# Optimization experiments

Measured on AMD Instinct MI355X. Metric: run time of the kernel, lower is better.

The kernel has to match this reference:

```python
import jax, jax.numpy as jnp
import numpy as np
from jax import lax

STRIDE = 2
PADDING = 3
NUM_ROW = 8192
NUM_COL = 8192
KH, KW = 7, 7


def setup_inputs() -> dict:
    key = jax.random.key(0)
    kx, kw_, kb = jax.random.split(key, 3)
    enc_x = jax.random.normal(kx, (NUM_ROW * NUM_COL,), dtype=jnp.float32)
    weight = jax.random.normal(kw_, (1, 1, KH, KW), dtype=jnp.float32)
    bias = jax.random.normal(kb, (1,), dtype=jnp.float32)
    return {
        "enc_x": enc_x,
        "weight": weight,
        "bias": bias,
        "num_row": NUM_ROW,
        "num_col": NUM_COL,
    }


def reference(enc_x, weight, bias, num_row, num_col):
    # enc_x is the flattened (packed) image vector of a num_row x num_col image.
    # The CKKS Conv2dFunction computes a plain single-channel cross-correlation
    # (same semantics as torch Conv2d, 1 in / 1 out channel) + scalar bias,
    # returning the flattened output vector.
    x = enc_x.reshape(1, 1, num_row, num_col)  # NCHW
    out = lax.conv_general_dilated(
        x,
        weight,  # OIHW
        window_strides=(STRIDE, STRIDE),
        padding=[(PADDING, PADDING), (PADDING, PADDING)],
        dimension_numbers=("NCHW", "OIHW", "NCHW"),
    )
    out = out + bias[0]
    return out.reshape(-1)  # flattened, matching ciphertext packing
```

## Files before the change

kernel.cpp:

```cpp
#include <hip/hip_runtime.h>


#define THREADS 256
#define TILE_W 128
#define TILE_H 16
#define IN_H 37
#define CHUNKS 66
#define LDS_STRIDE (CHUNKS * 4)
#define NSLOT (IN_H * CHUNKS)
#define NSLOT_PAD 2560
#define IMG 8192
#define OUTW 4096

typedef __attribute__((address_space(1))) const void global_cv;
typedef __attribute__((address_space(3))) void lds_v;

__global__ __launch_bounds__(THREADS, 4)
void conv7x7_s2(const float* __restrict__ x, const float* __restrict__ wgt,
                const float* __restrict__ bias, float* __restrict__ out) {
  __shared__ __align__(16) float lds[NSLOT_PAD * 4];
  const int t = threadIdx.x;
  const int tile_x = blockIdx.x * TILE_W;
  const int tile_y = blockIdx.y * TILE_H;
  const int g0c4 = tile_x * 2 - 4;
  const int g0r = tile_y * 2 - 3;

  float wv[49];
#pragma unroll
  for (int i = 0; i < 49; ++i) wv[i] = wgt[i];
  const float bv = bias[0];

  const bool interior = (blockIdx.x >= 1) & (blockIdx.x <= 30) &
                        (blockIdx.y >= 1) & (blockIdx.y <= 254);

  if (interior) {
    const float* xb = x + (long long)g0r * IMG + g0c4;
#pragma unroll
    for (int i = 0; i < 10; ++i) {
      const int s = t + THREADS * i;
      const int r = s / CHUNKS;
      const int q = s - r * CHUNKS;
      const int xr = (r >> 2) & 7;
      const int src = (q < 64) ? (q ^ xr) : q;
      const float* gp = xb + r * IMG + 4 * src;
      if (i == 9 && s >= NSLOT) gp = x;
      __builtin_amdgcn_global_load_lds((global_cv*)gp, (lds_v*)&lds[s * 4],
                                       16, 0, 0);
    }
  } else {
    float4 vbuf[10];
    int laddr[10];
#pragma unroll
    for (int i = 0; i < 10; ++i) {
      const int s = t + THREADS * i;
      const bool ok = (s < NSLOT);
      const int r = s / CHUNKS;
      const int q = s - r * CHUNKS;
      const int xr = (r >> 2) & 7;
      const int src = (q < 64) ? (q ^ xr) : q;
      const int gr = g0r + r;
      const int gc = g0c4 + 4 * src;
      float4 v = make_float4(0.f, 0.f, 0.f, 0.f);
      if (ok && (unsigned)gr < (unsigned)IMG && (unsigned)gc < (unsigned)(IMG - 3))
        v = *reinterpret_cast<const float4*>(&x[(long long)gr * IMG + gc]);
      vbuf[i] = v;
      laddr[i] = ok ? s * 4 : -1;
    }
#pragma unroll
    for (int i = 0; i < 10; ++i)
      if (laddr[i] >= 0) *reinterpret_cast<float4*>(&lds[laddr[i]]) = vbuf[i];
  }
  __syncthreads();

  const int tx = t & 31;
  const int ty = t >> 5;
  float acc[2][4];
#pragma unroll
  for (int y = 0; y < 2; ++y)
#pragma unroll
    for (int xx = 0; xx < 4; ++xx) acc[y][xx] = bv;

#pragma unroll
  for (int j = 0; j < 9; ++j) {
    const int sl = 4 * ty + j;
    const int xr = (sl >> 2) & 7;
    float rbuf[16];
#pragma unroll
    for (int q = 0; q < 4; ++q) {
      const int c = 2 * tx + q;
      const int lq = (c < 64) ? (c ^ xr) : c;
      const float4 v =
          *reinterpret_cast<const float4*>(&lds[sl * LDS_STRIDE + lq * 4]);
      rbuf[4 * q + 0] = v.x;
      rbuf[4 * q + 1] = v.y;
      rbuf[4 * q + 2] = v.z;
      rbuf[4 * q + 3] = v.w;
    }
#pragma unroll
    for (int y = 0; y < 2; ++y) {
      const int kh = j - 2 * y;
      if (kh >= 0 && kh <= 6) {
#pragma unroll
        for (int xx = 0; xx < 4; ++xx)
#pragma unroll
          for (int kw = 0; kw < 7; ++kw)
            acc[y][xx] = fmaf(rbuf[2 * xx + kw + 1], wv[kh * 7 + kw], acc[y][xx]);
      }
    }
  }

  const int ox = tile_x + 4 * tx;
  const int oy = tile_y + 2 * ty;
#pragma unroll
  for (int y = 0; y < 2; ++y) {
    float4 v = make_float4(acc[y][0], acc[y][1], acc[y][2], acc[y][3]);
    *reinterpret_cast<float4*>(&out[(long long)(oy + y) * OUTW + ox]) = v;
  }
}

extern "C" void kernel_launch(void* const* d_in, const int* in_sizes, int n_in,
                              void* d_out, int out_size, void* d_ws, size_t ws_size,
                              hipStream_t stream) {
  const float* x = (const float*)d_in[0];
  const float* w = (const float*)d_in[1];
  const float* b = (const float*)d_in[2];
  float* out = (float*)d_out;
  dim3 grid(OUTW / TILE_W, OUTW / TILE_H);
  conv7x7_s2<<<grid, dim3(THREADS), 0, stream>>>(x, w, b, out);
}
```

Baseline: 67.00 us.

## Widen conv tile to 256x8 and store LDS chunks even/odd split

Changes the output tile from 128x16 to 256x8 per block, which shrinks the input halo rows loaded per block (21 rows instead of 37 for half as many output rows) and widens each row. The LDS layout replaces the XOR swizzle with a split of even and odd 16-byte chunks into separate halves of each row, so each thread's four float4 reads are consecutive across lanes and avoid bank conflicts without swizzle arithmetic. LDS use per block grows and the occupancy hint drops from 4 to 3 blocks per SIMD-group, trading some latency hiding for less redundant halo traffic.

```diff
diff --git a/kernel.cpp b/kernel.cpp
--- a/kernel.cpp
+++ b/kernel.cpp
@@ -2,20 +2,21 @@
 
 
 #define THREADS 256
-#define TILE_W 128
-#define TILE_H 16
-#define IN_H 37
-#define CHUNKS 66
-#define LDS_STRIDE (CHUNKS * 4)
+#define TILE_W 256
+#define TILE_H 8
+#define IN_H 21
+#define CHUNKS 130
+#define ROWF (CHUNKS * 4)
 #define NSLOT (IN_H * CHUNKS)
-#define NSLOT_PAD 2560
+#define NROUND 11
+#define NSLOT_PAD (NROUND * THREADS)
 #define IMG 8192
 #define OUTW 4096
 
 typedef __attribute__((address_space(1))) const void global_cv;
 typedef __attribute__((address_space(3))) void lds_v;
 
-__global__ __launch_bounds__(THREADS, 4)
+__global__ __launch_bounds__(THREADS, 3)
 void conv7x7_s2(const float* __restrict__ x, const float* __restrict__ wgt,
                 const float* __restrict__ bias, float* __restrict__ out) {
   __shared__ __align__(16) float lds[NSLOT_PAD * 4];
@@ -30,34 +31,32 @@
   for (int i = 0; i < 49; ++i) wv[i] = wgt[i];
   const float bv = bias[0];
 
-  const bool interior = (blockIdx.x >= 1) & (blockIdx.x <= 30) &
-                        (blockIdx.y >= 1) & (blockIdx.y <= 254);
+  const bool interior = (blockIdx.x >= 1) & (blockIdx.x <= 14) &
+                        (blockIdx.y >= 1) & (blockIdx.y <= 510);
 
   if (interior) {
     const float* xb = x + (long long)g0r * IMG + g0c4;
 #pragma unroll
-    for (int i = 0; i < 10; ++i) {
+    for (int i = 0; i < NROUND; ++i) {
       const int s = t + THREADS * i;
       const int r = s / CHUNKS;
-      const int q = s - r * CHUNKS;
-      const int xr = (r >> 2) & 7;
-      const int src = (q < 64) ? (q ^ xr) : q;
+      const int p = s - r * CHUNKS;
+      const int src = (p < 65) ? (2 * p) : (2 * (p - 65) + 1);
       const float* gp = xb + r * IMG + 4 * src;
-      if (i == 9 && s >= NSLOT) gp = x;
+      if (i == NROUND - 1 && s >= NSLOT) gp = x;
       __builtin_amdgcn_global_load_lds((global_cv*)gp, (lds_v*)&lds[s * 4],
                                        16, 0, 0);
     }
   } else {
-    float4 vbuf[10];
-    int laddr[10];
+    float4 vbuf[NROUND];
+    int laddr[NROUND];
 #pragma unroll
-    for (int i = 0; i < 10; ++i) {
+    for (int i = 0; i < NROUND; ++i) {
       const int s = t + THREADS * i;
       const bool ok = (s < NSLOT);
       const int r = s / CHUNKS;
-      const int q = s - r * CHUNKS;
-      const int xr = (r >> 2) & 7;
-      const int src = (q < 64) ? (q ^ xr) : q;
+      const int p = s - r * CHUNKS;
+      const int src = (p < 65) ? (2 * p) : (2 * (p - 65) + 1);
       const int gr = g0r + r;
       const int gc = g0c4 + 4 * src;
       float4 v = make_float4(0.f, 0.f, 0.f, 0.f);
@@ -67,13 +66,13 @@
       laddr[i] = ok ? s * 4 : -1;
     }
 #pragma unroll
-    for (int i = 0; i < 10; ++i)
+    for (int i = 0; i < NROUND; ++i)
       if (laddr[i] >= 0) *reinterpret_cast<float4*>(&lds[laddr[i]]) = vbuf[i];
   }
   __syncthreads();
 
-  const int tx = t & 31;
-  const int ty = t >> 5;
+  const int tx = t & 63;
+  const int ty = t >> 6;
   float acc[2][4];
 #pragma unroll
   for (int y = 0; y < 2; ++y)
@@ -83,18 +82,17 @@
 #pragma unroll
   for (int j = 0; j < 9; ++j) {
     const int sl = 4 * ty + j;
-    const int xr = (sl >> 2) & 7;
+    const float* rp = &lds[sl * ROWF];
     float rbuf[16];
-#pragma unroll
-    for (int q = 0; q < 4; ++q) {
-      const int c = 2 * tx + q;
-      const int lq = (c < 64) ? (c ^ xr) : c;
-      const float4 v =
-          *reinterpret_cast<const float4*>(&lds[sl * LDS_STRIDE + lq * 4]);
-      rbuf[4 * q + 0] = v.x;
-      rbuf[4 * q + 1] = v.y;
-      rbuf[4 * q + 2] = v.z;
-      rbuf[4 * q + 3] = v.w;
+    {
+      const float4 v0 = *reinterpret_cast<const float4*>(rp + (tx) * 4);
+      const float4 v1 = *reinterpret_cast<const float4*>(rp + (65 + tx) * 4);
+      const float4 v2 = *reinterpret_cast<const float4*>(rp + (tx + 1) * 4);
+      const float4 v3 = *reinterpret_cast<const float4*>(rp + (66 + tx) * 4);
+      rbuf[0] = v0.x;  rbuf[1] = v0.y;  rbuf[2] = v0.z;  rbuf[3] = v0.w;
+      rbuf[4] = v1.x;  rbuf[5] = v1.y;  rbuf[6] = v1.z;  rbuf[7] = v1.w;
+      rbuf[8] = v2.x;  rbuf[9] = v2.y;  rbuf[10] = v2.z; rbuf[11] = v2.w;
+      rbuf[12] = v3.x; rbuf[13] = v3.y; rbuf[14] = v3.z; rbuf[15] = v3.w;
     }
 #pragma unroll
     for (int y = 0; y < 2; ++y) {
```

After: 65.52 us. -2.2%, faster.
